# Kernel tuning notes

Hardware: AMD Instinct MI355X
Metric: run time of the kernel (lower is better)

The kernel has to match this reference:

```python
import jax, jax.numpy as jnp
import numpy as np

BIG = 1e9  # finite 'null' sentinel standing in for +inf (min / shortest-path DP)


def _minplus_scan(a, c):
    """Solve v[j] = min(c[j], v[j-1] + a[j]) along last axis (v[0] = c[0] when a[0]=BIG).
    Min-plus linear recurrence -> associative scan over pairs (a, c)."""
    def combine(x, y):
        a1, c1 = x
        a2, c2 = y
        return a1 + a2, jnp.minimum(c2, c1 + a2)
    _, v = jax.lax.associative_scan(combine, (a, c), axis=-1)
    return v


def setup_inputs() -> dict:
    key = jax.random.key(0)
    images = jax.random.uniform(key, (2048, 64, 64), dtype=jnp.float32)
    return {"images": images}


def reference(images):
    # Grid DAG on HxW nodes; edges (i,j-1)->(i,j), (i-1,j)->(i,j), (i-1,j-1)->(i,j).
    # GraphLayer: edge potential theta(u->v) = (img[u] + img[v]) / 2.
    # SPFunction: shortest-path DP from (0,0) to (H-1,W-1); returns path length per sample.
    B, H, W = images.shape
    img = images
    t_right = 0.5 * (img[:, :, :-1] + img[:, :, 1:])      # [B, H,   W-1]
    t_down  = 0.5 * (img[:, :-1, :] + img[:, 1:, :])      # [B, H-1, W  ]
    t_diag  = 0.5 * (img[:, :-1, :-1] + img[:, 1:, 1:])   # [B, H-1, W-1]

    # Row 0: only right edges -> plain cumulative sum.
    d0 = jnp.concatenate(
        [jnp.zeros((B, 1), dtype=img.dtype), jnp.cumsum(t_right[:, 0, :], axis=-1)],
        axis=-1,
    )  # [B, W]

    a_pad = jnp.full((B, 1), jnp.float32(BIG), dtype=img.dtype)

    def row_step(prev, xs):
        td, tdg, tr = xs  # td: [B,W], tdg: [B,W-1], tr: [B,W-1]
        c = prev + td                                  # candidate via down edge
        diag_cand = prev[:, :-1] + tdg                 # candidate via diag edge
        c = c.at[:, 1:].set(jnp.minimum(c[:, 1:], diag_cand))
        a = jnp.concatenate([a_pad, tr], axis=-1)      # right-edge weights, a[0]=BIG
        v = _minplus_scan(a, c)                        # fold in right edges within the row
        return v, None

    xs = (
        jnp.moveaxis(t_down, 1, 0),            # [H-1, B, W]
        jnp.moveaxis(t_diag, 1, 0),            # [H-1, B, W-1]
        jnp.moveaxis(t_right[:, 1:, :], 1, 0), # [H-1, B, W-1]
    )
    d_last, _ = jax.lax.scan(row_step, d0, xs)
    return d_last[:, -1]  # [B] shortest-path lengths
```

## Files before the change

kernel.cpp:

```cpp
#include <hip/hip_runtime.h>

#define BIG 1e9f

__device__ __forceinline__ float dpp_shr1_big(float src) {
    return __int_as_float(__builtin_amdgcn_update_dpp(
        __float_as_int(BIG), __float_as_int(src),
        0x138 , 0xF, 0xF, false));
}

__global__ __launch_bounds__(128) void dp_diag_kernel(const float* __restrict__ img,
                                                      float* __restrict__ out, int B) {
    __shared__ float smem[2][4096];
    const int lane = threadIdx.x & 63;
    const int wave = threadIdx.x >> 6;
    const int b = (blockIdx.x << 1) + wave;
    const bool active = (b < B);

    float* s = smem[wave];
    if (active) {
        const float4* g4 = (const float4*)(img + ((size_t)b << 12));
        float4* s4 = (float4*)s;
        #pragma unroll
        for (int t = 0; t < 16; ++t)
            s4[(t << 6) + lane] = g4[(t << 6) + lane];
    }
    __syncthreads();

    if (active) {
        auto rd = [&](int k) -> float {
            int i  = k - lane;
            int ic = i < 0 ? 0 : (i > 63 ? 63 : i);
            return s[(ic << 6) | lane];
        };

        float e  = (lane == 0) ? 0.5f * s[0] : BIG;
        float xs = BIG;

        auto step = [&](float w) {
            float x = dpp_shr1_big(e);
            float m = fminf(fminf(x, e), xs);
            e  = m + w;
            xs = x;
        };

        float pf0 = rd(1), pf1 = rd(2), pf2 = rd(3), pf3 = rd(4);
        float pf4 = rd(5), pf5 = rd(6), pf6 = rd(7), pf7 = rd(8);

        int k = 1;
        #pragma unroll 1
        for (int g = 0; g < 15; ++g, k += 8) {
            float h0 = pf0, h1 = pf1, h2 = pf2, h3 = pf3;
            float h4 = pf4, h5 = pf5, h6 = pf6, h7 = pf7;
            pf0 = rd(k + 8);  pf1 = rd(k + 9);  pf2 = rd(k + 10); pf3 = rd(k + 11);
            pf4 = rd(k + 12); pf5 = rd(k + 13); pf6 = rd(k + 14); pf7 = rd(k + 15);
            step(h0); step(h1); step(h2); step(h3);
            step(h4); step(h5); step(h6); step(h7);
        }
        step(pf0); step(pf1); step(pf2); step(pf3); step(pf4); step(pf5);

        if (lane == 63) out[b] = e - 0.5f * s[4095];
    }
}

extern "C" void kernel_launch(void* const* d_in, const int* in_sizes, int n_in,
                              void* d_out, int out_size, void* d_ws, size_t ws_size,
                              hipStream_t stream) {
    const float* img = (const float*)d_in[0];
    float* out = (float*)d_out;
    const int B = out_size;
    const int threads = 128;
    const int grid = (B + 1) / 2;
    dp_diag_kernel<<<grid, threads, 0, stream>>>(img, out, B);
}
```

Measured before the change: 74.28 us.

## Hand-schedule anti-diagonal DP loop in inline assembly with deep LDS prefetch ring

```diff
diff --git a/kernel.cpp b/kernel.cpp
--- a/kernel.cpp
+++ b/kernel.cpp
@@ -2,64 +2,87 @@
 
 #define BIG 1e9f
 
-__device__ __forceinline__ float dpp_shr1_big(float src) {
-    return __int_as_float(__builtin_amdgcn_update_dpp(
-        __float_as_int(BIG), __float_as_int(src),
-        0x138 , 0xF, 0xF, false));
-}
+#define RD(W) \
+    "v_add_u32 %[ik], 1, %[ik]\n\t" \
+    "v_med3_i32 %[ic], %[ik], 0, 63\n\t" \
+    "v_lshl_add_u32 %[ad], %[ic], 8, %[sb]\n\t" \
+    "ds_read_b32 " W ", %[ad]\n\t"
+
+#define CMP(W, XN, XO) \
+    "s_waitcnt lgkmcnt(12)\n\t" \
+    "v_mov_b32 " XN ", %[vbig]\n\t" \
+    "v_mov_b32_dpp " XN ", %[e] wave_shr:1 row_mask:0xf bank_mask:0xf\n\t" \
+    "v_min3_f32 %[tp], " XN ", %[e], " XO "\n\t" \
+    "v_add_f32 %[e], %[tp], " W "\n\t"
+
+#define SLOT(WISS, WCON, XN, XO) RD(WISS) CMP(WCON, XN, XO)
 
 __global__ __launch_bounds__(128) void dp_diag_kernel(const float* __restrict__ img,
                                                       float* __restrict__ out, int B) {
-    __shared__ float smem[2][4096];
+    __shared__ __align__(16) float smem[2][4096];
     const int lane = threadIdx.x & 63;
     const int wave = threadIdx.x >> 6;
     const int b = (blockIdx.x << 1) + wave;
-    const bool active = (b < B);
+    if (b >= B) return;
 
     float* s = smem[wave];
-    if (active) {
+    {
         const float4* g4 = (const float4*)(img + ((size_t)b << 12));
         float4* s4 = (float4*)s;
         #pragma unroll
         for (int t = 0; t < 16; ++t)
             s4[(t << 6) + lane] = g4[(t << 6) + lane];
     }
-    __syncthreads();
 
-    if (active) {
-        auto rd = [&](int k) -> float {
-            int i  = k - lane;
-            int ic = i < 0 ? 0 : (i > 63 ? 63 : i);
-            return s[(ic << 6) | lane];
-        };
+    float e  = (lane == 0) ? 0.5f * s[0] : BIG;
+    float x0 = BIG, x1 = BIG;
+    float w0 = 0, w1 = 0, w2 = 0, w3 = 0, w4 = 0, w5 = 0, w6 = 0,
+          w7 = 0, w8 = 0, w9 = 0, w10 = 0, w11 = 0, w12 = 0, w13 = 0;
+    int ik = -lane;
+    int ic = 0; unsigned ad = 0; float tp = 0;
+    const float    vbig  = BIG;
+    const unsigned sbase = (unsigned)(uintptr_t)s + ((unsigned)lane << 2);
 
-        float e  = (lane == 0) ? 0.5f * s[0] : BIG;
-        float xs = BIG;
+    asm volatile(
+        RD("%[w1]") RD("%[w2]") RD("%[w3]") RD("%[w4]") RD("%[w5]") RD("%[w6]")
+        RD("%[w7]") RD("%[w8]") RD("%[w9]") RD("%[w10]") RD("%[w11]") RD("%[w12]")
+        "s_nop 2\n\t"
+        : [ik]"+v"(ik), [ic]"+v"(ic), [ad]"+v"(ad),
+          [w1]"+v"(w1), [w2]"+v"(w2), [w3]"+v"(w3), [w4]"+v"(w4),
+          [w5]"+v"(w5), [w6]"+v"(w6), [w7]"+v"(w7), [w8]"+v"(w8),
+          [w9]"+v"(w9), [w10]"+v"(w10), [w11]"+v"(w11), [w12]"+v"(w12)
+        : [sb]"v"(sbase)
+        : "memory");
 
-        auto step = [&](float w) {
-            float x = dpp_shr1_big(e);
-            float m = fminf(fminf(x, e), xs);
-            e  = m + w;
-            xs = x;
-        };
+    #pragma unroll 1
+    for (int it = 0; it < 9; ++it) {
+        asm volatile(
+            SLOT("%[w13]", "%[w1]",  "%[x0]", "%[x1]")
+            SLOT("%[w0]",  "%[w2]",  "%[x1]", "%[x0]")
+            SLOT("%[w1]",  "%[w3]",  "%[x0]", "%[x1]")
+            SLOT("%[w2]",  "%[w4]",  "%[x1]", "%[x0]")
+            SLOT("%[w3]",  "%[w5]",  "%[x0]", "%[x1]")
+            SLOT("%[w4]",  "%[w6]",  "%[x1]", "%[x0]")
+            SLOT("%[w5]",  "%[w7]",  "%[x0]", "%[x1]")
+            SLOT("%[w6]",  "%[w8]",  "%[x1]", "%[x0]")
+            SLOT("%[w7]",  "%[w9]",  "%[x0]", "%[x1]")
+            SLOT("%[w8]",  "%[w10]", "%[x1]", "%[x0]")
+            SLOT("%[w9]",  "%[w11]", "%[x0]", "%[x1]")
+            SLOT("%[w10]", "%[w12]", "%[x1]", "%[x0]")
+            SLOT("%[w11]", "%[w13]", "%[x0]", "%[x1]")
+            SLOT("%[w12]", "%[w0]",  "%[x1]", "%[x0]")
+            : [e]"+v"(e), [x0]"+v"(x0), [x1]"+v"(x1), [tp]"+v"(tp),
+              [ik]"+v"(ik), [ic]"+v"(ic), [ad]"+v"(ad),
+              [w0]"+v"(w0), [w1]"+v"(w1), [w2]"+v"(w2), [w3]"+v"(w3),
+              [w4]"+v"(w4), [w5]"+v"(w5), [w6]"+v"(w6), [w7]"+v"(w7),
+              [w8]"+v"(w8), [w9]"+v"(w9), [w10]"+v"(w10), [w11]"+v"(w11),
+              [w12]"+v"(w12), [w13]"+v"(w13)
+            : [sb]"v"(sbase), [vbig]"v"(vbig)
+            : "memory");
+    }
+    asm volatile("s_waitcnt lgkmcnt(0)\n\t" ::: "memory");
 
-        float pf0 = rd(1), pf1 = rd(2), pf2 = rd(3), pf3 = rd(4);
-        float pf4 = rd(5), pf5 = rd(6), pf6 = rd(7), pf7 = rd(8);
-
-        int k = 1;
-        #pragma unroll 1
-        for (int g = 0; g < 15; ++g, k += 8) {
-            float h0 = pf0, h1 = pf1, h2 = pf2, h3 = pf3;
-            float h4 = pf4, h5 = pf5, h6 = pf6, h7 = pf7;
-            pf0 = rd(k + 8);  pf1 = rd(k + 9);  pf2 = rd(k + 10); pf3 = rd(k + 11);
-            pf4 = rd(k + 12); pf5 = rd(k + 13); pf6 = rd(k + 14); pf7 = rd(k + 15);
-            step(h0); step(h1); step(h2); step(h3);
-            step(h4); step(h5); step(h6); step(h7);
-        }
-        step(pf0); step(pf1); step(pf2); step(pf3); step(pf4); step(pf5);
-
-        if (lane == 63) out[b] = e - 0.5f * s[4095];
-    }
+    if (lane == 63) out[b] = e - 0.5f * s[4095];
 }
 
 extern "C" void kernel_launch(void* const* d_in, const int* in_sizes, int n_in,
```

New measurement: 73.50 us. About the same (-1.0%).
